# Kernel optimization log

Hardware: AMD Instinct MI355X
Metric: run time of the kernel (lower is better)

Reference implementation:

```python
import jax, jax.numpy as jnp
import numpy as np

NUM_TOKENS = 4096
HIDDEN = 2048
INTER = 1408
NUM_EXPERTS = 8
TOP_K = 2


def setup_inputs() -> dict:
    key = jax.random.key(0)
    k1, k2, k3, k4, k5 = jax.random.split(key, 5)
    hidden_states = jax.random.normal(k1, (NUM_TOKENS, HIDDEN), dtype=jnp.float32)
    # w1: (E, 2*I, H) gate+up fused; w2: (E, H, I)
    w1 = jax.random.normal(k2, (NUM_EXPERTS, 2 * INTER, HIDDEN), dtype=jnp.float32) * (1.0 / np.sqrt(HIDDEN))
    w2 = jax.random.normal(k3, (NUM_EXPERTS, HIDDEN, INTER), dtype=jnp.float32) * (1.0 / np.sqrt(INTER))
    raw = jax.random.uniform(k4, (NUM_TOKENS, TOP_K), dtype=jnp.float32)
    topk_weights = raw / jnp.sum(raw, axis=-1, keepdims=True)  # router softmax-normalized weights
    topk_ids = jax.random.randint(k5, (NUM_TOKENS, TOP_K), 0, NUM_EXPERTS, dtype=jnp.int32)
    return {"hidden_states": hidden_states, "w1": w1, "w2": w2,
            "topk_weights": topk_weights, "topk_ids": topk_ids}


def reference(hidden_states, w1, w2, topk_weights, topk_ids):
    """Math-equivalent of fused_experts (dispatch -> grouped gate_up GEMM ->
    SwiGLU -> grouped down GEMM -> weighted scatter-combine).

    Expressed densely per expert (E is small and fixed), which yields the
    identical output to the sorted/grouped-GEMM formulation.
    """
    E = w1.shape[0]
    inter = w1.shape[1] // 2
    dtype = hidden_states.dtype
    # gate_up projection for every expert: [E, N, 2I]
    gate_up = jnp.einsum('nh,eih->eni', hidden_states, w1)
    gate, up = gate_up[..., :inter], gate_up[..., inter:]
    act = jax.nn.silu(gate) * up  # npu_swiglu: silu(first half) * second half
    # down projection: [E, N, H]
    expert_out = jnp.einsum('eni,ehi->enh', act, w2)
    # combine weight per (token, expert): sum of topk_weights where routed
    one_hot = jax.nn.one_hot(topk_ids, E, dtype=dtype)          # [N, K, E]
    combine = jnp.sum(topk_weights[:, :, None] * one_hot, axis=1)  # [N, E]
    return jnp.einsum('ne,enh->nh', combine, expert_out)
```

## Files before the change

kernel.cpp:

```cpp
#include <hip/hip_runtime.h>
#include <hip/hip_bf16.h>

#define NTOK 4096
#define HID 2048
#define INTER 1408
#define NEXP 8
#define NPAIR 8192
#define NKT1 32
#define NKT2 22
#define SZ2 16384

typedef short bf16x8 __attribute__((ext_vector_type(8)));
typedef float f32x4 __attribute__((ext_vector_type(4)));

__device__ __forceinline__ unsigned short f2bf(float f) {
  unsigned u = __builtin_bit_cast(unsigned, f);
  u += 0x7fffu + ((u >> 16) & 1u);
  return (unsigned short)(u >> 16);
}
__device__ __forceinline__ float bf2f(unsigned short v) {
  return __builtin_bit_cast(float, (unsigned)v << 16);
}

__device__ __forceinline__ void gload16(const void* g, void* l) {
  __builtin_amdgcn_global_load_lds(
      (const __attribute__((address_space(1))) void*)g,
      (__attribute__((address_space(3))) void*)l, 16, 0, 0);
}

__device__ __forceinline__ int xcd_swz(int lin, int nwg) {
  int xcd = lin & 7, base = lin >> 3;
  int q = nwg >> 3, r = nwg & 7;
  return (xcd < r ? xcd * (q + 1) : r * (q + 1) + (xcd - r) * q) + base;
}

#define BAR __builtin_amdgcn_s_barrier()
#define SCHED0 __builtin_amdgcn_sched_barrier(0)
#define LGKM0 asm volatile("s_waitcnt lgkmcnt(0)" ::: "memory")
#define VM6 asm volatile("s_waitcnt vmcnt(6)" ::: "memory")
#define VM4 asm volatile("s_waitcnt vmcnt(4)" ::: "memory")
#define VM0 asm volatile("s_waitcnt vmcnt(0)" ::: "memory")
#define PRIO1 __builtin_amdgcn_s_setprio(1)
#define PRIO0 __builtin_amdgcn_s_setprio(0)

__global__ void k_cvt_all(const float* __restrict__ hs, const float* __restrict__ w1,
                          const float* __restrict__ w2, unsigned short* __restrict__ dst) {
  const int N0 = NTOK * HID / 4;
  const int N1 = N0 + NEXP * 2 * INTER * HID / 4;
  const int N2 = N1 + NEXP * HID * INTER / 4;
  int i = blockIdx.x * blockDim.x + threadIdx.x;
  int stride = gridDim.x * blockDim.x;
  for (; i < N2; i += stride) {
    const float* s; int o;
    if (i < N0) { s = hs; o = i; }
    else if (i < N1) { s = w1; o = i - N0; }
    else { s = w2; o = i - N1; }
    float4 v = reinterpret_cast<const float4*>(s)[o];
    ushort4 u;
    u.x = f2bf(v.x); u.y = f2bf(v.y); u.z = f2bf(v.z); u.w = f2bf(v.w);
    reinterpret_cast<ushort4*>(dst)[i] = u;
  }
}

__global__ void k_route(const int* __restrict__ ids, int* __restrict__ ctrl,
                        unsigned short* __restrict__ row_token,
                        unsigned short* __restrict__ inv_row) {
  __shared__ int cnt[NEXP], cur[NEXP];
  int t = threadIdx.x;
  if (t < NEXP) cnt[t] = 0;
  __syncthreads();
  for (int p = t; p < NPAIR; p += 512) atomicAdd(&cnt[ids[p]], 1);
  __syncthreads();
  if (t == 0) {
    int acc = 0, T1 = 0, T2 = 0;
    for (int e = 0; e < NEXP; ++e) {
      cur[e] = acc;
      ctrl[e] = cnt[e];
      ctrl[8 + e] = acc;
      int n1 = (cnt[e] + 255) >> 8;
      for (int m = 0; m < n1; ++m) { ctrl[32 + T1] = e; ctrl[71 + T1] = m; ++T1; }
      int n2 = (cnt[e] + 127) >> 7;
      for (int m = 0; m < n2; ++m) { ctrl[110 + T2] = e; ctrl[181 + T2] = m; ++T2; }
      acc += cnt[e];
    }
    ctrl[16] = T1;
    ctrl[17] = T2;
  }
  __syncthreads();
  for (int p = t; p < NPAIR; p += 512) {
    int e = ids[p];
    int pos = atomicAdd(&cur[e], 1);
    row_token[pos] = (unsigned short)(p >> 1);
    inv_row[p] = (unsigned short)pos;
  }
}


#define G1_STAGE_A(BB, u, ktile) \
  gload16(asrc[(u)*2+0] + (ktile)*64, lds + (BB) + ((u)*2+0)*4096 + wvb); \
  gload16(asrc[(u)*2+1] + (ktile)*64, lds + (BB) + ((u)*2+1)*4096 + wvb);
#define G1_STAGE_B(BB, u, ktile) \
  gload16(bsrc[(u)*2+0] + (ktile)*64, lds + (BB) + 16384 + ((u)*2+0)*4096 + wvb); \
  gload16(bsrc[(u)*2+1] + (ktile)*64, lds + (BB) + 16384 + ((u)*2+1)*4096 + wvb);

#define G1_READ_A(dst, BB, mh) \
  _Pragma("unroll") for (int m_ = 0; m_ < 4; ++m_) { \
    dst[m_][0] = *(const bf16x8*)(lds + (BB) + aoff + (mh)*8192 + m_*1024 + csw0); \
    dst[m_][1] = *(const bf16x8*)(lds + (BB) + aoff + (mh)*8192 + m_*1024 + csw1); \
  }
#define G1_READ_B(dst, BB, nh) \
  _Pragma("unroll") for (int n_ = 0; n_ < 2; ++n_) { \
    dst[n_][0] = *(const bf16x8*)(lds + (BB) + boff + (nh)*8192 + n_*1024 + csw0); \
    dst[n_][1] = *(const bf16x8*)(lds + (BB) + boff + (nh)*8192 + n_*1024 + csw1); \
  }

#define G1_MMA_Q(afr, bfr, mh, nh) \
  _Pragma("unroll") for (int m_ = 0; m_ < 4; ++m_) \
  _Pragma("unroll") for (int n_ = 0; n_ < 2; ++n_) { \
    acc[(mh)*4+m_][(nh)*2+n_] = __builtin_amdgcn_mfma_f32_16x16x32_bf16(afr[m_][0], bfr[n_][0], acc[(mh)*4+m_][(nh)*2+n_], 0, 0, 0); \
    acc[(mh)*4+m_][(nh)*2+n_] = __builtin_amdgcn_mfma_f32_16x16x32_bf16(afr[m_][1], bfr[n_][1], acc[(mh)*4+m_][(nh)*2+n_], 0, 0, 0); \
  }

#define G1_EIGHT(kt) \
  G1_READ_A(afM0, 0, 0) G1_READ_B(bfN0, 0, 0) G1_STAGE_B(32768, 1, (kt)+1); \
  BAR; LGKM0; PRIO1; G1_MMA_Q(afM0, bfN0, 0, 0) PRIO0; BAR; \
  G1_READ_B(bfN1, 0, 1) G1_STAGE_B(0, 0, (kt)+2); \
  BAR; LGKM0; PRIO1; G1_MMA_Q(afM0, bfN1, 0, 1) PRIO0; BAR; \
  G1_READ_A(afM1, 0, 1) G1_STAGE_A(0, 0, (kt)+2); \
  BAR; LGKM0; PRIO1; G1_MMA_Q(afM1, bfN1, 1, 1) PRIO0; BAR; \
  G1_STAGE_A(0, 1, (kt)+2); \
  BAR; LGKM0; PRIO1; G1_MMA_Q(afM1, bfN0, 1, 0) PRIO0; VM6; BAR; \
  G1_READ_A(afM0, 32768, 0) G1_READ_B(bfN0, 32768, 0) G1_STAGE_B(0, 1, (kt)+2); \
  BAR; LGKM0; PRIO1; G1_MMA_Q(afM0, bfN0, 0, 0) PRIO0; BAR; \
  G1_READ_B(bfN1, 32768, 1) G1_STAGE_B(32768, 0, (kt)+3); \
  BAR; LGKM0; PRIO1; G1_MMA_Q(afM0, bfN1, 0, 1) PRIO0; BAR; \
  G1_READ_A(afM1, 32768, 1) G1_STAGE_A(32768, 0, (kt)+3); \
  BAR; LGKM0; PRIO1; G1_MMA_Q(afM1, bfN1, 1, 1) PRIO0; BAR; \
  G1_STAGE_A(32768, 1, (kt)+3); \
  BAR; LGKM0; PRIO1; G1_MMA_Q(afM1, bfN0, 1, 0) PRIO0; VM6; BAR;

#define G1_EPI(kt) \
  G1_READ_A(afM0, 0, 0) G1_READ_B(bfN0, 0, 0) G1_STAGE_B(32768, 1, (kt)+1); \
  BAR; LGKM0; PRIO1; G1_MMA_Q(afM0, bfN0, 0, 0) PRIO0; BAR; \
  G1_READ_B(bfN1, 0, 1) \
  BAR; LGKM0; PRIO1; G1_MMA_Q(afM0, bfN1, 0, 1) PRIO0; BAR; \
  G1_READ_A(afM1, 0, 1) \
  BAR; LGKM0; PRIO1; G1_MMA_Q(afM1, bfN1, 1, 1) PRIO0; BAR; \
  BAR; LGKM0; PRIO1; G1_MMA_Q(afM1, bfN0, 1, 0) PRIO0; VM0; BAR; \
  G1_READ_A(afM0, 32768, 0) G1_READ_B(bfN0, 32768, 0) \
  BAR; LGKM0; PRIO1; G1_MMA_Q(afM0, bfN0, 0, 0) PRIO0; BAR; \
  G1_READ_B(bfN1, 32768, 1) \
  BAR; LGKM0; PRIO1; G1_MMA_Q(afM0, bfN1, 0, 1) PRIO0; BAR; \
  G1_READ_A(afM1, 32768, 1) \
  BAR; LGKM0; PRIO1; G1_MMA_Q(afM1, bfN1, 1, 1) PRIO0; BAR; \
  LGKM0; PRIO1; G1_MMA_Q(afM1, bfN0, 1, 0) PRIO0;

__global__ __launch_bounds__(512, 2) void k_gemm1(
    const unsigned short* __restrict__ hs,
    const unsigned short* __restrict__ w1,
    const int* __restrict__ ctrl,
    const unsigned short* __restrict__ row_token,
    unsigned short* __restrict__ act) {
  const int T1 = ctrl[16];
  const int nwg = T1 * 11;
  const int lin = blockIdx.x;
  if (lin >= nwg) return;
  const int wg = xcd_swz(lin, nwg);
  const int ti = wg / 11;
  const int nt = wg - ti * 11;
  const int e = ctrl[32 + ti], mt = ctrl[71 + ti];
  const int rows = ctrl[e], off_e = ctrl[8 + e];
  const int n0g = nt * 128;
  const unsigned short* w1e = w1 + (size_t)e * (2 * INTER * HID);

  __shared__ unsigned short smem[65536];
  unsigned short* lds = smem;

  const int t = threadIdx.x;
  const int lane = t & 63, wv = t >> 6;
  const int wm = wv >> 2, wn = wv & 3;
  const int lm = lane & 15, hi4 = lane >> 4;
  const int wvb = (t & 448) * 8;
  const int aoff = (wm * 64 + lm) * 64;
  const int boff = 16384 + (wn * 32 + lm) * 64;
  const int csw0 = (hi4 ^ (lm & 7)) * 8;
  const int csw1 = ((4 + hi4) ^ (lm & 7)) * 8;

  const unsigned short* asrc[4];
#pragma unroll
  for (int i = 0; i < 4; ++i) {
    int p = i * 64 + (t >> 3);
    int r = ((p >> 6) & 1) * 128 + (p >> 7) * 64 + (p & 63);
    int grow = mt * 256 + r;
    if (grow > rows - 1) grow = rows - 1;
    int token = row_token[off_e + grow];
    asrc[i] = hs + (size_t)token * HID + ((t & 7) ^ (p & 7)) * 8;
  }
  const unsigned short* bsrc[4];
#pragma unroll
  for (int i = 0; i < 4; ++i) {
    int p = i * 64 + (t >> 3);
    int nh = p >> 7, wns = (p & 127) >> 5, idx = p & 31;
    int c = n0g + wns * 32 + idx + nh * INTER;
    bsrc[i] = w1e + (size_t)c * HID + ((t & 7) ^ (p & 7)) * 8;
  }

  f32x4 acc[8][4];
#pragma unroll
  for (int i = 0; i < 8; ++i)
#pragma unroll
    for (int j = 0; j < 4; ++j) acc[i][j] = (f32x4){0.f, 0.f, 0.f, 0.f};
  bf16x8 afM0[4][2], afM1[4][2], bfN0[2][2], bfN1[2][2];

  G1_STAGE_B(0, 0, 0) G1_STAGE_A(0, 0, 0) G1_STAGE_A(0, 1, 0) G1_STAGE_B(0, 1, 0)
  G1_STAGE_B(32768, 0, 1) G1_STAGE_A(32768, 0, 1) G1_STAGE_A(32768, 1, 1)
  VM6; BAR;

  for (int kt = 0; kt + 3 < NKT1; kt += 2) { G1_EIGHT(kt) }
  G1_EPI(NKT1 - 2)

#pragma unroll
  for (int mh = 0; mh < 2; ++mh)
#pragma unroll
    for (int m = 0; m < 4; ++m)
#pragma unroll
      for (int n = 0; n < 2; ++n) {
        int col = n0g + wn * 32 + n * 16 + lm;
#pragma unroll
        for (int j = 0; j < 4; ++j) {
          int grow = mt * 256 + wm * 128 + mh * 64 + m * 16 + hi4 * 4 + j;
          if (grow < rows) {
            float g = acc[mh * 4 + m][n][j];
            float u = acc[mh * 4 + m][2 + n][j];
            float a = g / (1.0f + __expf(-g)) * u;
            act[(size_t)(off_e + grow) * INTER + col] = f2bf(a);
          }
        }
      }
}

#define G2_RD_A(BB) { \
  _Pragma("unroll") for (int m_ = 0; m_ < 4; ++m_) { \
    af[m_][0] = *(const bf16x8*)(smem + (BB) + aoff + m_*1024 + csw0); \
    af[m_][1] = *(const bf16x8*)(smem + (BB) + aoff + m_*1024 + csw1); } }
#define G2_RD_B(BB) { \
  _Pragma("unroll") for (int n_ = 0; n_ < 2; ++n_) { \
    bfr[n_][0] = *(const bf16x8*)(smem + (BB) + boff + n_*1024 + csw0); \
    bfr[n_][1] = *(const bf16x8*)(smem + (BB) + boff + n_*1024 + csw1); } }

__global__ __launch_bounds__(512, 4) void k_gemm2(
    const unsigned short* __restrict__ act,
    const unsigned short* __restrict__ w2,
    const int* __restrict__ ctrl,
    unsigned short* __restrict__ eo) {
  const int T2 = ctrl[17];
  const int nwg = T2 * 16;
  const int lin = blockIdx.x;
  if (lin >= nwg) return;
  const int wg = xcd_swz(lin, nwg);
  const int ti = wg >> 4;
  const int nt = wg & 15;
  const int e = ctrl[110 + ti], mt = ctrl[181 + ti];
  const int rows = ctrl[e], off_e = ctrl[8 + e];
  const int n0 = nt * 128;
  const unsigned short* w2e = w2 + (size_t)e * (HID * INTER);

  __shared__ unsigned short smem[SZ2 * 2];

  const int t = threadIdx.x;
  const int lane = t & 63, wv = t >> 6;
  const int wm = wv >> 2, wn = wv & 3;
  const int lm = lane & 15, hi4 = lane >> 4;
  const int aoff = (wm * 64 + lm) * 64;
  const int boff = 8192 + (wn * 32 + lm) * 64;
  const int csw0 = (hi4 ^ (lm & 7)) * 8;
  const int csw1 = ((4 + hi4) ^ (lm & 7)) * 8;
  const int ldst = t * 8;

  const unsigned short* asrc[2];
#pragma unroll
  for (int i = 0; i < 2; ++i) {
    int p = i * 512 + t;
    int row = p >> 3, c = p & 7;
    int grow = mt * 128 + row;
    if (grow > rows - 1) grow = rows - 1;
    asrc[i] = act + (size_t)(off_e + grow) * INTER + (c ^ (row & 7)) * 8;
  }
  const unsigned short* bsrc[2];
#pragma unroll
  for (int i = 0; i < 2; ++i) {
    int p = i * 512 + t;
    int cb = p >> 3, c = p & 7;
    bsrc[i] = w2e + (size_t)(n0 + cb) * INTER + (c ^ (cb & 7)) * 8;
  }

#define G2_STAGE(BB, kt) { \
  gload16(asrc[0] + (size_t)(kt)*64, smem + (BB) + ldst); \
  gload16(asrc[1] + (size_t)(kt)*64, smem + (BB) + 4096 + ldst); \
  gload16(bsrc[0] + (size_t)(kt)*64, smem + (BB) + 8192 + ldst); \
  gload16(bsrc[1] + (size_t)(kt)*64, smem + (BB) + 12288 + ldst); }

  f32x4 acc[4][2];
#pragma unroll
  for (int m = 0; m < 4; ++m)
#pragma unroll
    for (int n = 0; n < 2; ++n) acc[m][n] = (f32x4){0.f, 0.f, 0.f, 0.f};
  bf16x8 af[4][2], bfr[2][2];

  G2_STAGE(0, 0)
  G2_STAGE(SZ2, 1)
  VM4; BAR;

  unsigned cur = 0, oth = SZ2;
  for (int kt = 0; kt < NKT2; ++kt) {
    G2_RD_A(cur)
    G2_RD_B(cur)
    LGKM0; BAR;
    SCHED0;
    if (kt + 2 < NKT2) { G2_STAGE(cur, kt + 2) }
    PRIO1;
#pragma unroll
    for (int kk = 0; kk < 2; ++kk)
#pragma unroll
      for (int m = 0; m < 4; ++m)
#pragma unroll
        for (int n = 0; n < 2; ++n)
          acc[m][n] = __builtin_amdgcn_mfma_f32_16x16x32_bf16(af[m][kk], bfr[n][kk], acc[m][n], 0, 0, 0);
    PRIO0;
    if (kt < NKT2 - 2) { VM4; BAR; }
    else if (kt == NKT2 - 2) { VM0; BAR; }
    unsigned tmp = cur; cur = oth; oth = tmp;
  }

#pragma unroll
  for (int m = 0; m < 4; ++m)
#pragma unroll
    for (int n = 0; n < 2; ++n) {
      int col = n0 + wn * 32 + n * 16 + lm;
#pragma unroll
      for (int j = 0; j < 4; ++j) {
        int grow = mt * 128 + wm * 64 + m * 16 + hi4 * 4 + j;
        if (grow < rows)
          eo[(size_t)(off_e + grow) * HID + col] = f2bf(acc[m][n][j]);
      }
    }
#undef G2_STAGE
}

__global__ void k_combine(const unsigned short* __restrict__ eo,
                          const float* __restrict__ tw,
                          const unsigned short* __restrict__ inv_row,
                          float* __restrict__ out) {
  int idx = blockIdx.x * blockDim.x + threadIdx.x;
  int tok = idx >> 8;
  int c8 = (idx & 255) * 8;
  int r0 = inv_row[tok * 2], r1 = inv_row[tok * 2 + 1];
  float w0 = tw[tok * 2], w1 = tw[tok * 2 + 1];
  bf16x8 v0 = *(const bf16x8*)(eo + (size_t)r0 * HID + c8);
  bf16x8 v1 = *(const bf16x8*)(eo + (size_t)r1 * HID + c8);
  float4 o0, o1;
  o0.x = w0 * bf2f((unsigned short)v0[0]) + w1 * bf2f((unsigned short)v1[0]);
  o0.y = w0 * bf2f((unsigned short)v0[1]) + w1 * bf2f((unsigned short)v1[1]);
  o0.z = w0 * bf2f((unsigned short)v0[2]) + w1 * bf2f((unsigned short)v1[2]);
  o0.w = w0 * bf2f((unsigned short)v0[3]) + w1 * bf2f((unsigned short)v1[3]);
  o1.x = w0 * bf2f((unsigned short)v0[4]) + w1 * bf2f((unsigned short)v1[4]);
  o1.y = w0 * bf2f((unsigned short)v0[5]) + w1 * bf2f((unsigned short)v1[5]);
  o1.z = w0 * bf2f((unsigned short)v0[6]) + w1 * bf2f((unsigned short)v1[6]);
  o1.w = w0 * bf2f((unsigned short)v0[7]) + w1 * bf2f((unsigned short)v1[7]);
  float4* op = reinterpret_cast<float4*>(out) + (size_t)tok * 512 + (idx & 255) * 2;
  op[0] = o0;
  op[1] = o1;
}

extern "C" void kernel_launch(void* const* d_in, const int* in_sizes, int n_in,
                              void* d_out, int out_size, void* d_ws, size_t ws_size,
                              hipStream_t stream) {
  const float* hs_f = (const float*)d_in[0];
  const float* w1_f = (const float*)d_in[1];
  const float* w2_f = (const float*)d_in[2];
  const float* tw   = (const float*)d_in[3];
  const int*   tids = (const int*)d_in[4];
  float* out = (float*)d_out;

  char* ws = (char*)d_ws;
  unsigned short* hs_b = (unsigned short*)(ws);
  unsigned short* w1_b = (unsigned short*)(ws + 16777216);
  unsigned short* w2_b = (unsigned short*)(ws + 109051904);
  unsigned short* act  = (unsigned short*)(ws + 155189248);
  unsigned short* eo   = (unsigned short*)(ws + 16777216);
  int* ctrl = (int*)(ws + 178257920);
  unsigned short* row_token = (unsigned short*)(ws + 178258944);
  unsigned short* inv_row   = (unsigned short*)(ws + 178275328);

  k_route<<<1, 512, 0, stream>>>(tids, ctrl, row_token, inv_row);
  k_cvt_all<<<4096, 256, 0, stream>>>(hs_f, w1_f, w2_f, hs_b);

  k_gemm1<<<39 * 11, 512, 0, stream>>>(hs_b, w1_b, ctrl, row_token, act);
  k_gemm2<<<71 * 16, 512, 0, stream>>>(act, w2_b, ctrl, eo);
  k_combine<<<NTOK * HID / 8 / 256, 256, 0, stream>>>(eo, tw, inv_row, out);
}
```

Measured before the change: 282.0 us.

## Shrink gemm1 tiles, merge routing into conversion, overlap w2 conversion with gemm1

Routing is merged into the hs/w1 conversion kernel as block 0, removing one launch. The w2 fp32-to-bf16 conversion moves into spare workgroups of k_gemm1 so it runs alongside the first GEMM. k_gemm1 is rewritten to use 128-row tiles with a simpler double-buffered K=32 loop, keeping separate gate and up accumulators, at 4 blocks per CU instead of 2. This gives more workgroups and fewer uneven tail tiles, but each workgroup reuses less data and has a shallower pipeline.

After: 260.7 us. -7.5%, faster.

```diff
diff --git a/kernel.cpp b/kernel.cpp
--- a/kernel.cpp
+++ b/kernel.cpp
@@ -6,8 +6,9 @@
 #define INTER 1408
 #define NEXP 8
 #define NPAIR 8192
-#define NKT1 32
+#define NK1 64
 #define NKT2 22
+#define G1SZ 24576
 #define SZ2 16384
 
 typedef short bf16x8 __attribute__((ext_vector_type(8)));
@@ -37,24 +38,51 @@
 #define BAR __builtin_amdgcn_s_barrier()
 #define SCHED0 __builtin_amdgcn_sched_barrier(0)
 #define LGKM0 asm volatile("s_waitcnt lgkmcnt(0)" ::: "memory")
-#define VM6 asm volatile("s_waitcnt vmcnt(6)" ::: "memory")
 #define VM4 asm volatile("s_waitcnt vmcnt(4)" ::: "memory")
+#define VM3 asm volatile("s_waitcnt vmcnt(3)" ::: "memory")
 #define VM0 asm volatile("s_waitcnt vmcnt(0)" ::: "memory")
 #define PRIO1 __builtin_amdgcn_s_setprio(1)
 #define PRIO0 __builtin_amdgcn_s_setprio(0)
 
-__global__ void k_cvt_all(const float* __restrict__ hs, const float* __restrict__ w1,
-                          const float* __restrict__ w2, unsigned short* __restrict__ dst) {
+__global__ void k_prep(const float* __restrict__ hs, const float* __restrict__ w1,
+                       unsigned short* __restrict__ dst,
+                       const int* __restrict__ ids, int* __restrict__ ctrl,
+                       unsigned short* __restrict__ row_token,
+                       unsigned short* __restrict__ inv_row) {
+  if (blockIdx.x == 0) {
+    __shared__ int cnt[NEXP], cur[NEXP];
+    int t = threadIdx.x;
+    if (t < NEXP) cnt[t] = 0;
+    __syncthreads();
+    for (int p = t; p < NPAIR; p += 512) atomicAdd(&cnt[ids[p]], 1);
+    __syncthreads();
+    if (t == 0) {
+      int acc = 0, T = 0;
+      for (int e = 0; e < NEXP; ++e) {
+        cur[e] = acc;
+        ctrl[e] = cnt[e];
+        ctrl[8 + e] = acc;
+        int n = (cnt[e] + 127) >> 7;
+        for (int m = 0; m < n; ++m) { ctrl[32 + T] = e; ctrl[104 + T] = m; ++T; }
+        acc += cnt[e];
+      }
+      ctrl[16] = T;
+    }
+    __syncthreads();
+    for (int p = t; p < NPAIR; p += 512) {
+      int e = ids[p];
+      int pos = atomicAdd(&cur[e], 1);
+      row_token[pos] = (unsigned short)(p >> 1);
+      inv_row[p] = (unsigned short)pos;
+    }
+    return;
+  }
   const int N0 = NTOK * HID / 4;
   const int N1 = N0 + NEXP * 2 * INTER * HID / 4;
-  const int N2 = N1 + NEXP * HID * INTER / 4;
-  int i = blockIdx.x * blockDim.x + threadIdx.x;
-  int stride = gridDim.x * blockDim.x;
-  for (; i < N2; i += stride) {
-    const float* s; int o;
-    if (i < N0) { s = hs; o = i; }
-    else if (i < N1) { s = w1; o = i - N0; }
-    else { s = w2; o = i - N1; }
+  int stride = (gridDim.x - 1) * 512;
+  for (int i = (blockIdx.x - 1) * 512 + threadIdx.x; i < N1; i += stride) {
+    const float* s = (i < N0) ? hs : w1;
+    int o = (i < N0) ? i : i - N0;
     float4 v = reinterpret_cast<const float4*>(s)[o];
     ushort4 u;
     u.x = f2bf(v.x); u.y = f2bf(v.y); u.z = f2bf(v.z); u.w = f2bf(v.w);
@@ -62,181 +90,118 @@
   }
 }
 
-__global__ void k_route(const int* __restrict__ ids, int* __restrict__ ctrl,
-                        unsigned short* __restrict__ row_token,
-                        unsigned short* __restrict__ inv_row) {
-  __shared__ int cnt[NEXP], cur[NEXP];
-  int t = threadIdx.x;
-  if (t < NEXP) cnt[t] = 0;
-  __syncthreads();
-  for (int p = t; p < NPAIR; p += 512) atomicAdd(&cnt[ids[p]], 1);
-  __syncthreads();
-  if (t == 0) {
-    int acc = 0, T1 = 0, T2 = 0;
-    for (int e = 0; e < NEXP; ++e) {
-      cur[e] = acc;
-      ctrl[e] = cnt[e];
-      ctrl[8 + e] = acc;
-      int n1 = (cnt[e] + 255) >> 8;
-      for (int m = 0; m < n1; ++m) { ctrl[32 + T1] = e; ctrl[71 + T1] = m; ++T1; }
-      int n2 = (cnt[e] + 127) >> 7;
-      for (int m = 0; m < n2; ++m) { ctrl[110 + T2] = e; ctrl[181 + T2] = m; ++T2; }
-      acc += cnt[e];
-    }
-    ctrl[16] = T1;
-    ctrl[17] = T2;
-  }
-  __syncthreads();
-  for (int p = t; p < NPAIR; p += 512) {
-    int e = ids[p];
-    int pos = atomicAdd(&cur[e], 1);
-    row_token[pos] = (unsigned short)(p >> 1);
-    inv_row[p] = (unsigned short)pos;
-  }
-}
-
-
-#define G1_STAGE_A(BB, u, ktile) \
-  gload16(asrc[(u)*2+0] + (ktile)*64, lds + (BB) + ((u)*2+0)*4096 + wvb); \
-  gload16(asrc[(u)*2+1] + (ktile)*64, lds + (BB) + ((u)*2+1)*4096 + wvb);
-#define G1_STAGE_B(BB, u, ktile) \
-  gload16(bsrc[(u)*2+0] + (ktile)*64, lds + (BB) + 16384 + ((u)*2+0)*4096 + wvb); \
-  gload16(bsrc[(u)*2+1] + (ktile)*64, lds + (BB) + 16384 + ((u)*2+1)*4096 + wvb);
-
-#define G1_READ_A(dst, BB, mh) \
-  _Pragma("unroll") for (int m_ = 0; m_ < 4; ++m_) { \
-    dst[m_][0] = *(const bf16x8*)(lds + (BB) + aoff + (mh)*8192 + m_*1024 + csw0); \
-    dst[m_][1] = *(const bf16x8*)(lds + (BB) + aoff + (mh)*8192 + m_*1024 + csw1); \
-  }
-#define G1_READ_B(dst, BB, nh) \
+
+#define G1_STAGE(BB, kt) { \
+  gload16(aptr + (size_t)(kt)*32, smem + (BB) + wvb16); \
+  gload16(bptr0 + (size_t)(kt)*32, smem + (BB) + 8192 + wvb16); \
+  gload16(bptr1 + (size_t)(kt)*32, smem + (BB) + 16384 + wvb16); }
+
+#define G1_RD(BB) { \
+  _Pragma("unroll") for (int m_ = 0; m_ < 4; ++m_) \
+    af[m_] = *(const bf16x8*)(smem + (BB) + arow + m_*1024 + swz); \
   _Pragma("unroll") for (int n_ = 0; n_ < 2; ++n_) { \
-    dst[n_][0] = *(const bf16x8*)(lds + (BB) + boff + (nh)*8192 + n_*1024 + csw0); \
-    dst[n_][1] = *(const bf16x8*)(lds + (BB) + boff + (nh)*8192 + n_*1024 + csw1); \
-  }
-
-#define G1_MMA_Q(afr, bfr, mh, nh) \
+    bg[n_] = *(const bf16x8*)(smem + (BB) + brow + n_*1024 + swz); \
+    bu[n_] = *(const bf16x8*)(smem + (BB) + brow + 8192 + n_*1024 + swz); } }
+
+#define G1_MMA \
   _Pragma("unroll") for (int m_ = 0; m_ < 4; ++m_) \
   _Pragma("unroll") for (int n_ = 0; n_ < 2; ++n_) { \
-    acc[(mh)*4+m_][(nh)*2+n_] = __builtin_amdgcn_mfma_f32_16x16x32_bf16(afr[m_][0], bfr[n_][0], acc[(mh)*4+m_][(nh)*2+n_], 0, 0, 0); \
-    acc[(mh)*4+m_][(nh)*2+n_] = __builtin_amdgcn_mfma_f32_16x16x32_bf16(afr[m_][1], bfr[n_][1], acc[(mh)*4+m_][(nh)*2+n_], 0, 0, 0); \
-  }
-
-#define G1_EIGHT(kt) \
-  G1_READ_A(afM0, 0, 0) G1_READ_B(bfN0, 0, 0) G1_STAGE_B(32768, 1, (kt)+1); \
-  BAR; LGKM0; PRIO1; G1_MMA_Q(afM0, bfN0, 0, 0) PRIO0; BAR; \
-  G1_READ_B(bfN1, 0, 1) G1_STAGE_B(0, 0, (kt)+2); \
-  BAR; LGKM0; PRIO1; G1_MMA_Q(afM0, bfN1, 0, 1) PRIO0; BAR; \
-  G1_READ_A(afM1, 0, 1) G1_STAGE_A(0, 0, (kt)+2); \
-  BAR; LGKM0; PRIO1; G1_MMA_Q(afM1, bfN1, 1, 1) PRIO0; BAR; \
-  G1_STAGE_A(0, 1, (kt)+2); \
-  BAR; LGKM0; PRIO1; G1_MMA_Q(afM1, bfN0, 1, 0) PRIO0; VM6; BAR; \
-  G1_READ_A(afM0, 32768, 0) G1_READ_B(bfN0, 32768, 0) G1_STAGE_B(0, 1, (kt)+2); \
-  BAR; LGKM0; PRIO1; G1_MMA_Q(afM0, bfN0, 0, 0) PRIO0; BAR; \
-  G1_READ_B(bfN1, 32768, 1) G1_STAGE_B(32768, 0, (kt)+3); \
-  BAR; LGKM0; PRIO1; G1_MMA_Q(afM0, bfN1, 0, 1) PRIO0; BAR; \
-  G1_READ_A(afM1, 32768, 1) G1_STAGE_A(32768, 0, (kt)+3); \
-  BAR; LGKM0; PRIO1; G1_MMA_Q(afM1, bfN1, 1, 1) PRIO0; BAR; \
-  G1_STAGE_A(32768, 1, (kt)+3); \
-  BAR; LGKM0; PRIO1; G1_MMA_Q(afM1, bfN0, 1, 0) PRIO0; VM6; BAR;
-
-#define G1_EPI(kt) \
-  G1_READ_A(afM0, 0, 0) G1_READ_B(bfN0, 0, 0) G1_STAGE_B(32768, 1, (kt)+1); \
-  BAR; LGKM0; PRIO1; G1_MMA_Q(afM0, bfN0, 0, 0) PRIO0; BAR; \
-  G1_READ_B(bfN1, 0, 1) \
-  BAR; LGKM0; PRIO1; G1_MMA_Q(afM0, bfN1, 0, 1) PRIO0; BAR; \
-  G1_READ_A(afM1, 0, 1) \
-  BAR; LGKM0; PRIO1; G1_MMA_Q(afM1, bfN1, 1, 1) PRIO0; BAR; \
-  BAR; LGKM0; PRIO1; G1_MMA_Q(afM1, bfN0, 1, 0) PRIO0; VM0; BAR; \
-  G1_READ_A(afM0, 32768, 0) G1_READ_B(bfN0, 32768, 0) \
-  BAR; LGKM0; PRIO1; G1_MMA_Q(afM0, bfN0, 0, 0) PRIO0; BAR; \
-  G1_READ_B(bfN1, 32768, 1) \
-  BAR; LGKM0; PRIO1; G1_MMA_Q(afM0, bfN1, 0, 1) PRIO0; BAR; \
-  G1_READ_A(afM1, 32768, 1) \
-  BAR; LGKM0; PRIO1; G1_MMA_Q(afM1, bfN1, 1, 1) PRIO0; BAR; \
-  LGKM0; PRIO1; G1_MMA_Q(afM1, bfN0, 1, 0) PRIO0;
-
-__global__ __launch_bounds__(512, 2) void k_gemm1(
+    accg[m_][n_] = __builtin_amdgcn_mfma_f32_16x16x32_bf16(af[m_], bg[n_], accg[m_][n_], 0, 0, 0); \
+    accu[m_][n_] = __builtin_amdgcn_mfma_f32_16x16x32_bf16(af[m_], bu[n_], accu[m_][n_], 0, 0, 0); }
+
+__global__ __launch_bounds__(512, 4) void k_gemm1(
     const unsigned short* __restrict__ hs,
     const unsigned short* __restrict__ w1,
+    const float* __restrict__ w2f,
+    unsigned short* __restrict__ w2b,
     const int* __restrict__ ctrl,
     const unsigned short* __restrict__ row_token,
     unsigned short* __restrict__ act) {
-  const int T1 = ctrl[16];
-  const int nwg = T1 * 11;
+  const int T = ctrl[16];
+  const int nwg = T * 11;
   const int lin = blockIdx.x;
-  if (lin >= nwg) return;
+  if (lin >= nwg) {
+    const int NW2 = NEXP * HID * INTER / 4;
+    int nc = gridDim.x - nwg;
+    for (int i = (lin - nwg) * 512 + threadIdx.x; i < NW2; i += nc * 512) {
+      float4 v = reinterpret_cast<const float4*>(w2f)[i];
+      ushort4 u;
+      u.x = f2bf(v.x); u.y = f2bf(v.y); u.z = f2bf(v.z); u.w = f2bf(v.w);
+      reinterpret_cast<ushort4*>(w2b)[i] = u;
+    }
+    return;
+  }
   const int wg = xcd_swz(lin, nwg);
   const int ti = wg / 11;
   const int nt = wg - ti * 11;
-  const int e = ctrl[32 + ti], mt = ctrl[71 + ti];
+  const int e = ctrl[32 + ti], mt = ctrl[104 + ti];
   const int rows = ctrl[e], off_e = ctrl[8 + e];
   const int n0g = nt * 128;
   const unsigned short* w1e = w1 + (size_t)e * (2 * INTER * HID);
 
-  __shared__ unsigned short smem[65536];
-  unsigned short* lds = smem;
+  __shared__ __align__(16) char smem[2 * G1SZ];
 
   const int t = threadIdx.x;
   const int lane = t & 63, wv = t >> 6;
   const int wm = wv >> 2, wn = wv & 3;
   const int lm = lane & 15, hi4 = lane >> 4;
-  const int wvb = (t & 448) * 8;
-  const int aoff = (wm * 64 + lm) * 64;
-  const int boff = 16384 + (wn * 32 + lm) * 64;
-  const int csw0 = (hi4 ^ (lm & 7)) * 8;
-  const int csw1 = ((4 + hi4) ^ (lm & 7)) * 8;
-
-  const unsigned short* asrc[4];
-#pragma unroll
-  for (int i = 0; i < 4; ++i) {
-    int p = i * 64 + (t >> 3);
-    int r = ((p >> 6) & 1) * 128 + (p >> 7) * 64 + (p & 63);
-    int grow = mt * 256 + r;
-    if (grow > rows - 1) grow = rows - 1;
-    int token = row_token[off_e + grow];
-    asrc[i] = hs + (size_t)token * HID + ((t & 7) ^ (p & 7)) * 8;
-  }
-  const unsigned short* bsrc[4];
-#pragma unroll
-  for (int i = 0; i < 4; ++i) {
-    int p = i * 64 + (t >> 3);
-    int nh = p >> 7, wns = (p & 127) >> 5, idx = p & 31;
-    int c = n0g + wns * 32 + idx + nh * INTER;
-    bsrc[i] = w1e + (size_t)c * HID + ((t & 7) ^ (p & 7)) * 8;
-  }
-
-  f32x4 acc[8][4];
-#pragma unroll
-  for (int i = 0; i < 8; ++i)
-#pragma unroll
-    for (int j = 0; j < 4; ++j) acc[i][j] = (f32x4){0.f, 0.f, 0.f, 0.f};
-  bf16x8 afM0[4][2], afM1[4][2], bfN0[2][2], bfN1[2][2];
-
-  G1_STAGE_B(0, 0, 0) G1_STAGE_A(0, 0, 0) G1_STAGE_A(0, 1, 0) G1_STAGE_B(0, 1, 0)
-  G1_STAGE_B(32768, 0, 1) G1_STAGE_A(32768, 0, 1) G1_STAGE_A(32768, 1, 1)
-  VM6; BAR;
-
-  for (int kt = 0; kt + 3 < NKT1; kt += 2) { G1_EIGHT(kt) }
-  G1_EPI(NKT1 - 2)
-
-#pragma unroll
-  for (int mh = 0; mh < 2; ++mh)
-#pragma unroll
-    for (int m = 0; m < 4; ++m)
-#pragma unroll
-      for (int n = 0; n < 2; ++n) {
-        int col = n0g + wn * 32 + n * 16 + lm;
-#pragma unroll
-        for (int j = 0; j < 4; ++j) {
-          int grow = mt * 256 + wm * 128 + mh * 64 + m * 16 + hi4 * 4 + j;
-          if (grow < rows) {
-            float g = acc[mh * 4 + m][n][j];
-            float u = acc[mh * 4 + m][2 + n][j];
-            float a = g / (1.0f + __expf(-g)) * u;
-            act[(size_t)(off_e + grow) * INTER + col] = f2bf(a);
-          }
+  const int wvb16 = (t & 448) * 16;
+  const int arow = wm * 4096 + lm * 64;
+  const int brow = 8192 + wn * 2048 + lm * 64;
+  const int swz = (hi4 ^ ((lm >> 1) & 3)) * 16;
+
+  const unsigned short *aptr, *bptr0, *bptr1;
+  {
+    int cl8 = ((t & 3) ^ ((t >> 3) & 3)) * 8;
+    int r = t >> 2;
+    int g0 = mt * 128 + r; if (g0 > rows - 1) g0 = rows - 1;
+    aptr = hs + (size_t)row_token[off_e + g0] * HID + cl8;
+    bptr0 = w1e + (size_t)(n0g + r) * HID + cl8;
+    bptr1 = w1e + (size_t)(INTER + n0g + r) * HID + cl8;
+  }
+
+  f32x4 accg[4][2], accu[4][2];
+#pragma unroll
+  for (int m = 0; m < 4; ++m)
+#pragma unroll
+    for (int n = 0; n < 2; ++n) {
+      accg[m][n] = (f32x4){0.f, 0.f, 0.f, 0.f};
+      accu[m][n] = (f32x4){0.f, 0.f, 0.f, 0.f};
+    }
+  bf16x8 af[4], bg[2], bu[2];
+
+  G1_STAGE(0, 0)
+  G1_STAGE(G1SZ, 1)
+  VM3; BAR;
+
+  unsigned cur = 0, oth = G1SZ;
+  for (int kt = 0; kt < NK1; ++kt) {
+    G1_RD(cur)
+    LGKM0; BAR;
+    SCHED0;
+    if (kt + 2 < NK1) { G1_STAGE(cur, kt + 2) }
+    PRIO1; G1_MMA PRIO0;
+    if (kt < NK1 - 2) { VM3; BAR; }
+    else if (kt == NK1 - 2) { VM0; BAR; }
+    unsigned tmp = cur; cur = oth; oth = tmp;
+  }
+
+#pragma unroll
+  for (int m = 0; m < 4; ++m)
+#pragma unroll
+    for (int n = 0; n < 2; ++n) {
+      int col = n0g + wn * 32 + n * 16 + lm;
+#pragma unroll
+      for (int j = 0; j < 4; ++j) {
+        int grow = mt * 128 + wm * 64 + m * 16 + hi4 * 4 + j;
+        if (grow < rows) {
+          float g = accg[m][n][j];
+          float u = accu[m][n][j];
+          float a = g / (1.0f + __expf(-g)) * u;
+          act[(size_t)(off_e + grow) * INTER + col] = f2bf(a);
         }
       }
+    }
 }
 
 #define G2_RD_A(BB) { \
@@ -253,14 +218,14 @@
     const unsigned short* __restrict__ w2,
     const int* __restrict__ ctrl,
     unsigned short* __restrict__ eo) {
-  const int T2 = ctrl[17];
-  const int nwg = T2 * 16;
+  const int T = ctrl[16];
+  const int nwg = T * 16;
   const int lin = blockIdx.x;
   if (lin >= nwg) return;
   const int wg = xcd_swz(lin, nwg);
   const int ti = wg >> 4;
   const int nt = wg & 15;
-  const int e = ctrl[110 + ti], mt = ctrl[181 + ti];
+  const int e = ctrl[32 + ti], mt = ctrl[104 + ti];
   const int rows = ctrl[e], off_e = ctrl[8 + e];
   const int n0 = nt * 128;
   const unsigned short* w2e = w2 + (size_t)e * (HID * INTER);
@@ -384,7 +349,6 @@
 
   char* ws = (char*)d_ws;
   unsigned short* hs_b = (unsigned short*)(ws);
-  unsigned short* w1_b = (unsigned short*)(ws + 16777216);
   unsigned short* w2_b = (unsigned short*)(ws + 109051904);
   unsigned short* act  = (unsigned short*)(ws + 155189248);
   unsigned short* eo   = (unsigned short*)(ws + 16777216);
@@ -392,10 +356,10 @@
   unsigned short* row_token = (unsigned short*)(ws + 178258944);
   unsigned short* inv_row   = (unsigned short*)(ws + 178275328);
 
-  k_route<<<1, 512, 0, stream>>>(tids, ctrl, row_token, inv_row);
-  k_cvt_all<<<4096, 256, 0, stream>>>(hs_f, w1_f, w2_f, hs_b);
-
-  k_gemm1<<<39 * 11, 512, 0, stream>>>(hs_b, w1_b, ctrl, row_token, act);
-  k_gemm2<<<71 * 16, 512, 0, stream>>>(act, w2_b, ctrl, eo);
+  k_prep<<<2049, 512, 0, stream>>>(hs_f, w1_f, hs_b, tids, ctrl, row_token, inv_row);
+
+  k_gemm1<<<1280, 512, 0, stream>>>(hs_b, (unsigned short*)(ws + 16777216), w2_f, w2_b,
+                                    ctrl, row_token, act);
+  k_gemm2<<<72 * 16, 512, 0, stream>>>(act, w2_b, ctrl, eo);
   k_combine<<<NTOK * HID / 8 / 256, 256, 0, stream>>>(eo, tw, inv_row, out);
 }
```
